# Kernel tuning notes

Hardware: AMD Instinct MI355X
Metric: run time of the kernel (lower is better)

The kernel has to match this reference:

```python
import jax, jax.numpy as jnp
import numpy as np

B, NQ, NP, C, H = 8, 1024, 2048, 1024, 16
D = C // H  # head_dim = 64


def setup_inputs() -> dict:
    key = jax.random.key(0)
    ks = jax.random.split(key, 12)
    s = 1.0 / np.sqrt(C)
    inp = {
        "x": jax.random.normal(ks[0], (B, NQ, C), dtype=jnp.float32),
        "ctx": jax.random.normal(ks[1], (B, NP, C), dtype=jnp.float32),
        "freqs_cis": jax.random.normal(ks[2], (NP, D // 2, 2), dtype=jnp.float32),
        "wq": jax.random.normal(ks[3], (C, C), dtype=jnp.float32) * s,
        "bq": jnp.zeros((C,), dtype=jnp.float32),
        "wk": jax.random.normal(ks[4], (C, C), dtype=jnp.float32) * s,
        "bk": jnp.zeros((C,), dtype=jnp.float32),
        "wv": jax.random.normal(ks[5], (C, C), dtype=jnp.float32) * s,
        "bv": jnp.zeros((C,), dtype=jnp.float32),
        "wo": jax.random.normal(ks[6], (C, C), dtype=jnp.float32) * s,
        "bo": jnp.zeros((C,), dtype=jnp.float32),
    }
    return inp


def _apply_rope(k, freqs_cis):
    # k: [B, Np, H, D]; freqs_cis: [Np, D//2, 2] (cos, sin)
    b, n, h, d = k.shape
    kp = k.reshape(b, n, h, d // 2, 2)  # adjacent-pair complex convention
    kr, ki = kp[..., 0], kp[..., 1]
    cos = freqs_cis[None, :, None, :, 0]
    sin = freqs_cis[None, :, None, :, 1]
    out_r = kr * cos - ki * sin
    out_i = kr * sin + ki * cos
    return jnp.stack([out_r, out_i], axis=-1).reshape(b, n, h, d)


def reference(x, ctx, freqs_cis, wq, bq, wk, bk, wv, bv, wo, bo):
    b, nq, c = x.shape
    npx = ctx.shape[1]
    q = (jnp.einsum('bsc,oc->bso', x, wq) + bq).reshape(b, nq, H, D)
    k = (jnp.einsum('bsc,oc->bso', ctx, wk) + bk).reshape(b, npx, H, D)
    v = (jnp.einsum('bsc,oc->bso', ctx, wv) + bv).reshape(b, npx, H, D)
    k = _apply_rope(k, freqs_cis)
    scale = 1.0 / jnp.sqrt(jnp.asarray(D, dtype=q.dtype))
    scores = jnp.einsum('bqhd,bkhd->bhqk', q, k) * scale
    attn = jax.nn.softmax(scores, axis=-1)
    out = jnp.einsum('bhqk,bkhd->bqhd', attn, v).reshape(b, nq, c)
    return jnp.einsum('bsc,oc->bso', out, wo) + bo
```

## Files before the change

### kernel.cpp

```cpp
#include <hip/hip_runtime.h>
#include <stdint.h>

typedef __bf16 bf16;
typedef bf16 bf16x8 __attribute__((ext_vector_type(8)));
typedef float f32x4 __attribute__((ext_vector_type(4)));
typedef float f32x16 __attribute__((ext_vector_type(16)));
typedef uint32_t u32x4 __attribute__((ext_vector_type(4)));

static __device__ __forceinline__ void async_cp16(const bf16* gsrc, bf16* ldst) {
  __builtin_amdgcn_global_load_lds(
      (const __attribute__((address_space(1))) uint32_t*)gsrc,
      (__attribute__((address_space(3))) uint32_t*)ldst, 16, 0, 0);
}

static __device__ __forceinline__ f32x16 mfma32(bf16x8 a, bf16x8 b, f32x16 c) {
  return __builtin_amdgcn_mfma_f32_32x32x16_bf16(a, b, c, 0, 0, 0);
}

static __device__ __forceinline__ uint32_t cvtpk(float lo, float hi) {
  uint32_t r;
  asm("v_cvt_pk_bf16_f32 %0, %1, %2" : "=v"(r) : "v"(lo), "v"(hi));
  return r;
}
static __device__ __forceinline__ void plswap(uint32_t& a, uint32_t& b) {
  asm("v_permlane32_swap_b32 %0, %1" : "+v"(a), "+v"(b));
}

__global__ __launch_bounds__(256) void convert_all(
    const float* __restrict__ x, const float* __restrict__ ctx,
    const float* __restrict__ wq, const float* __restrict__ wk,
    const float* __restrict__ wv, const float* __restrict__ wo,
    bf16* __restrict__ xb, bf16* __restrict__ cb,
    bf16* __restrict__ wqb, bf16* __restrict__ wkb,
    bf16* __restrict__ wvb, bf16* __restrict__ wob) {
  int id = blockIdx.x;
  const float* s; bf16* d; int base;
  if (id < 8192)        { s = x;   d = xb;  base = id; }
  else if (id < 24576)  { s = ctx; d = cb;  base = id - 8192; }
  else if (id < 25600)  { s = wq;  d = wqb; base = id - 24576; }
  else if (id < 26624)  { s = wk;  d = wkb; base = id - 25600; }
  else if (id < 27648)  { s = wv;  d = wvb; base = id - 26624; }
  else                  { s = wo;  d = wob; base = id - 27648; }
  int i = base * 256 + threadIdx.x;
  float4 v = ((const float4*)s)[i];
  ushort4 o;
  o.x = __builtin_bit_cast(unsigned short, (bf16)v.x);
  o.y = __builtin_bit_cast(unsigned short, (bf16)v.y);
  o.z = __builtin_bit_cast(unsigned short, (bf16)v.z);
  o.w = __builtin_bit_cast(unsigned short, (bf16)v.w);
  ((ushort4*)d)[i] = o;
}

template <int OUT_F32>
__global__ __launch_bounds__(256) void gemm_bt(
    const bf16* __restrict__ A, const bf16* __restrict__ Bw,
    const float* __restrict__ bias, void* __restrict__ Cout,
    int M, int N, int K) {
  __shared__ __align__(16) bf16 sA[128 * 32];
  __shared__ __align__(16) bf16 sB[128 * 32];

  int per = gridDim.x >> 3;
  int id = blockIdx.x;
  int swz = (id & 7) * per + (id >> 3);
  int NB = N >> 7;
  int mb = swz / NB, nb = swz % NB;

  int t = threadIdx.x;
  int l = t & 63, w = t >> 6;
  int wr = (w >> 1) * 64, wc = (w & 1) * 64;
  int lr = l & 15, lk = (l >> 4) * 8;

  const bf16* Abase = A + (size_t)(mb * 128 + (t >> 2)) * K + (t & 3) * 8;
  const bf16* Bbase = Bw + (size_t)(nb * 128 + (t >> 2)) * K + (t & 3) * 8;
  bf16* ldsA = sA + w * 512;
  bf16* ldsB = sB + w * 512;

  f32x4 acc[4][4];
  for (int i = 0; i < 4; i++)
    for (int j = 0; j < 4; j++) acc[i][j] = f32x4{0.f, 0.f, 0.f, 0.f};

  for (int k0 = 0; k0 < K; k0 += 32) {
    async_cp16(Abase + k0, ldsA);
    async_cp16(Abase + k0 + (size_t)64 * K, ldsA + 2048);
    async_cp16(Bbase + k0, ldsB);
    async_cp16(Bbase + k0 + (size_t)64 * K, ldsB + 2048);
    __syncthreads();
    bf16x8 af[4], bfr[4];
    for (int mf = 0; mf < 4; mf++)
      af[mf] = *(const bf16x8*)&sA[(wr + mf * 16 + lr) * 32 + lk];
    for (int nf = 0; nf < 4; nf++)
      bfr[nf] = *(const bf16x8*)&sB[(wc + nf * 16 + lr) * 32 + lk];
    for (int mf = 0; mf < 4; mf++)
      for (int nf = 0; nf < 4; nf++)
        acc[mf][nf] = __builtin_amdgcn_mfma_f32_16x16x32_bf16(
            af[mf], bfr[nf], acc[mf][nf], 0, 0, 0);
    __syncthreads();
  }

  int row0 = mb * 128 + wr + (l >> 4) * 4;
  int col0 = nb * 128 + wc + lr;
  for (int nf = 0; nf < 4; nf++) {
    float bi = bias[col0 + nf * 16];
    for (int mf = 0; mf < 4; mf++)
      for (int j = 0; j < 4; j++) {
        int r = row0 + mf * 16 + j;
        int c = col0 + nf * 16;
        float v = acc[mf][nf][j] + bi;
        if (OUT_F32)
          ((float*)Cout)[(size_t)r * N + c] = v;
        else
          ((bf16*)Cout)[(size_t)r * N + c] = (bf16)v;
      }
  }
}

__global__ __launch_bounds__(256) void rope_k(bf16* __restrict__ kb,
                                              const float* __restrict__ freqs) {
  int g = blockIdx.x * 256 + threadIdx.x;
  int c8 = g & 7;
  int n = (g >> 7) & 2047;
  uint4 kv = ((const uint4*)kb)[g];
  const float* f = freqs + n * 64 + c8 * 8;
  float4 f0 = *(const float4*)f;
  float4 f1 = *(const float4*)(f + 4);
  float cs[4] = {f0.x, f0.z, f1.x, f1.z};
  float sn[4] = {f0.y, f0.w, f1.y, f1.z};
  sn[3] = f1.w;
  unsigned short* ks = (unsigned short*)&kv;
  uint4 out;
  unsigned short* os = (unsigned short*)&out;
  for (int p = 0; p < 4; p++) {
    float kr = (float)__builtin_bit_cast(bf16, ks[2 * p]);
    float ki = (float)__builtin_bit_cast(bf16, ks[2 * p + 1]);
    float orr = kr * cs[p] - ki * sn[p];
    float oii = kr * sn[p] + ki * cs[p];
    os[2 * p] = __builtin_bit_cast(unsigned short, (bf16)orr);
    os[2 * p + 1] = __builtin_bit_cast(unsigned short, (bf16)oii);
  }
  ((uint4*)kb)[g] = out;
}

__global__ __launch_bounds__(256) void attn_fwd(
    const bf16* __restrict__ Q, const bf16* __restrict__ Kb,
    const bf16* __restrict__ Vb, bf16* __restrict__ O) {
  __shared__ __align__(16) bf16 sK[2][4096];
  __shared__ __align__(16) bf16 sV[2][4096];

  int nblk = blockIdx.x;
  int bh = (nblk & 7) * 16 + (nblk >> 6);
  int qt = (nblk >> 3) & 7;
  int b = bh >> 4, h = bh & 15;

  int t = threadIdx.x, l = t & 63, w = t >> 6;
  int ln = l & 31, hi = l >> 5;

  int qg = qt * 128 + w * 32 + ln;
  const bf16* qp = Q + ((size_t)(b * 1024 + qg) * 16 + h) * 64 + hi * 8;
  bf16x8 qf[4];
#pragma unroll
  for (int ds = 0; ds < 4; ds++) qf[ds] = *(const bf16x8*)(qp + ds * 16);

  const bf16* kbase = Kb + ((size_t)b * 2048 * 16 + h) * 64;
  const bf16* vbase = Vb + ((size_t)b * 2048 * 16 + h) * 64;

  int krow = w * 8 + (l >> 3);
  int vr2 = t >> 3;
  int vc = t & 7;

  auto stageK = [&](int kv0, int nb) {
    int cg1 = (((l & 7) ^ (krow & 7) ^ ((krow >> 3) & 7))) * 8;
    int r2 = krow + 32;
    int cg2 = (((l & 7) ^ (r2 & 7) ^ ((r2 >> 3) & 7))) * 8;
    async_cp16(kbase + (size_t)(kv0 + krow) * 1024 + cg1, &sK[nb][w * 512]);
    async_cp16(kbase + (size_t)(kv0 + r2) * 1024 + cg2, &sK[nb][2048 + w * 512]);
  };

  uint4 vA, vB;
  auto loadV = [&](int kv0) {
    const bf16* s = vbase + (size_t)(kv0 + 2 * vr2) * 1024 + vc * 8;
    vA = *(const uint4*)s;
    vB = *(const uint4*)(s + 1024);
  };
  auto writeV = [&](int nb) {
    const uint32_t* a0 = (const uint32_t*)&vA;
    const uint32_t* a1 = (const uint32_t*)&vB;
#pragma unroll
    for (int i = 0; i < 8; i++) {
      uint32_t lo = (a0[i >> 1] >> ((i & 1) * 16)) & 0xffffu;
      uint32_t hw = (a1[i >> 1] >> ((i & 1) * 16)) & 0xffffu;
      int d = vc * 8 + i;
      int off = d * 64 + ((2 * vr2) ^ ((i ^ vc) << 3));
      *(uint32_t*)&sV[nb][off] = lo | (hw << 16);
    }
  };

  f32x16 o0, o1, s0, s1;
#pragma unroll
  for (int i = 0; i < 16; i++) { o0[i] = 0.f; o1[i] = 0.f; }
  float m_r = -1e30f, l_r = 0.f;
  const float K2 = 0.18033688011112042f;

  stageK(0, 0);
  loadV(0);
  writeV(0);
  __syncthreads();
  int cur = 0;

  int x0 = ((ln & 7) ^ (ln >> 3)) << 3;
  int x1 = x0 ^ (4 << 3);

  for (int tt = 0; tt < 32; tt++) {
    if (tt < 31) { stageK(tt * 64 + 64, cur ^ 1); loadV(tt * 64 + 64); }

#pragma unroll
    for (int i = 0; i < 16; i++) { s0[i] = 0.f; s1[i] = 0.f; }
    __builtin_amdgcn_s_setprio(1);
#pragma unroll
    for (int ds = 0; ds < 4; ds++) {
      int boff = ds * 16 + hi * 8;
      bf16x8 kf0 = *(const bf16x8*)&sK[cur][ln * 64 + (boff ^ x0)];
      bf16x8 kf1 = *(const bf16x8*)&sK[cur][(ln + 32) * 64 + (boff ^ x1)];
      s0 = mfma32(kf0, qf[ds], s0);
      s1 = mfma32(kf1, qf[ds], s1);
    }
    __builtin_amdgcn_s_setprio(0);

    float mx[16];
#pragma unroll
    for (int i = 0; i < 16; i++) mx[i] = fmaxf(s0[i], s1[i]);
#pragma unroll
    for (int st = 8; st >= 1; st >>= 1)
#pragma unroll
      for (int i = 0; i < st; i++) mx[i] = fmaxf(mx[i], mx[i + st]);
    float pmax = fmaxf(mx[0], __shfl_xor(mx[0], 32, 64));

    if (__any(pmax > m_r + 40.f)) {
      float mnew = fmaxf(m_r, pmax);
      float corr = __builtin_amdgcn_exp2f((m_r - mnew) * K2);
      m_r = mnew;
      l_r *= corr;
#pragma unroll
      for (int i = 0; i < 16; i++) { o0[i] *= corr; o1[i] *= corr; }
    }
    float mk = m_r * K2;
    float sm[16];
#pragma unroll
    for (int i = 0; i < 16; i++) {
      s0[i] = __builtin_amdgcn_exp2f(__builtin_fmaf(s0[i], K2, -mk));
      s1[i] = __builtin_amdgcn_exp2f(__builtin_fmaf(s1[i], K2, -mk));
      sm[i] = s0[i] + s1[i];
    }
#pragma unroll
    for (int st = 8; st >= 1; st >>= 1)
#pragma unroll
      for (int i = 0; i < st; i++) sm[i] += sm[i + st];
    l_r += sm[0] + __shfl_xor(sm[0], 32, 64);

    bf16x8 pa[4];
    auto mkfrags = [&](const f32x16& sv, int base) {
#pragma unroll
      for (int u = 0; u < 2; u++) {
        uint32_t w0a = cvtpk(sv[8 * u + 0], sv[8 * u + 1]);
        uint32_t w0b = cvtpk(sv[8 * u + 4], sv[8 * u + 5]);
        plswap(w0a, w0b);
        uint32_t w1a = cvtpk(sv[8 * u + 2], sv[8 * u + 3]);
        uint32_t w1b = cvtpk(sv[8 * u + 6], sv[8 * u + 7]);
        plswap(w1a, w1b);
        u32x4 tmp;
        tmp[0] = w0a; tmp[1] = w1a; tmp[2] = w0b; tmp[3] = w1b;
        pa[base + u] = __builtin_bit_cast(bf16x8, tmp);
      }
    };
    mkfrags(s0, 0);
    mkfrags(s1, 2);

    __builtin_amdgcn_s_setprio(1);
#pragma unroll
    for (int ks = 0; ks < 4; ks++) {
      int koff = ks * 16 + hi * 8;
      bf16x8 vf0 = *(const bf16x8*)&sV[cur][ln * 64 + (koff ^ x0)];
      bf16x8 vf1 = *(const bf16x8*)&sV[cur][(ln + 32) * 64 + (koff ^ x1)];
      o0 = mfma32(vf0, pa[ks], o0);
      o1 = mfma32(vf1, pa[ks], o1);
    }
    __builtin_amdgcn_s_setprio(0);

    if (tt < 31) writeV(cur ^ 1);
    __syncthreads();
    cur ^= 1;
  }

  float inv = __builtin_amdgcn_rcpf(l_r);
  bf16* obase = O + ((size_t)(b * 1024 + qt * 128 + w * 32 + ln) * 16 + h) * 64;
#pragma unroll
  for (int g = 0; g < 4; g++) {
    ushort4 p0, p1;
    p0.x = __builtin_bit_cast(unsigned short, (bf16)(o0[4 * g + 0] * inv));
    p0.y = __builtin_bit_cast(unsigned short, (bf16)(o0[4 * g + 1] * inv));
    p0.z = __builtin_bit_cast(unsigned short, (bf16)(o0[4 * g + 2] * inv));
    p0.w = __builtin_bit_cast(unsigned short, (bf16)(o0[4 * g + 3] * inv));
    p1.x = __builtin_bit_cast(unsigned short, (bf16)(o1[4 * g + 0] * inv));
    p1.y = __builtin_bit_cast(unsigned short, (bf16)(o1[4 * g + 1] * inv));
    p1.z = __builtin_bit_cast(unsigned short, (bf16)(o1[4 * g + 2] * inv));
    p1.w = __builtin_bit_cast(unsigned short, (bf16)(o1[4 * g + 3] * inv));
    *(ushort4*)&obase[8 * g + 4 * hi] = p0;
    *(ushort4*)&obase[32 + 8 * g + 4 * hi] = p1;
  }
}

extern "C" void kernel_launch(void* const* d_in, const int* in_sizes, int n_in,
                              void* d_out, int out_size, void* d_ws, size_t ws_size,
                              hipStream_t stream) {
  const float* x     = (const float*)d_in[0];
  const float* ctx   = (const float*)d_in[1];
  const float* freqs = (const float*)d_in[2];
  const float* wq    = (const float*)d_in[3];
  const float* bq    = (const float*)d_in[4];
  const float* wk    = (const float*)d_in[5];
  const float* bk    = (const float*)d_in[6];
  const float* wv    = (const float*)d_in[7];
  const float* bv    = (const float*)d_in[8];
  const float* wo    = (const float*)d_in[9];
  const float* bo    = (const float*)d_in[10];

  char* p = (char*)d_ws;
  bf16* xb  = (bf16*)p; p += (size_t)8192 * 1024 * 2;
  bf16* cb  = (bf16*)p; p += (size_t)16384 * 1024 * 2;
  bf16* wqb = (bf16*)p; p += (size_t)1024 * 1024 * 2;
  bf16* wkb = (bf16*)p; p += (size_t)1024 * 1024 * 2;
  bf16* wvb = (bf16*)p; p += (size_t)1024 * 1024 * 2;
  bf16* wob = (bf16*)p; p += (size_t)1024 * 1024 * 2;
  bf16* qb  = (bf16*)p; p += (size_t)8192 * 1024 * 2;
  bf16* kb  = (bf16*)p; p += (size_t)16384 * 1024 * 2;
  bf16* vb  = (bf16*)p; p += (size_t)16384 * 1024 * 2;
  bf16* ob  = xb;

  convert_all<<<28672, 256, 0, stream>>>(x, ctx, wq, wk, wv, wo,
                                         xb, cb, wqb, wkb, wvb, wob);
  gemm_bt<0><<<512, 256, 0, stream>>>(xb, wqb, bq, qb, 8192, 1024, 1024);
  gemm_bt<0><<<1024, 256, 0, stream>>>(cb, wkb, bk, kb, 16384, 1024, 1024);
  gemm_bt<0><<<1024, 256, 0, stream>>>(cb, wvb, bv, vb, 16384, 1024, 1024);
  rope_k<<<8192, 256, 0, stream>>>(kb, freqs);
  attn_fwd<<<1024, 256, 0, stream>>>(qb, kb, vb, ob);
  gemm_bt<1><<<512, 256, 0, stream>>>(ob, wob, bo, d_out, 8192, 1024, 1024);
}
```

Baseline: 332.8 us.

## Produce V transposed from projection GEMM and stage it asynchronously in attention

The V projection GEMM now computes Wv·ctxᵀ, so V is written transposed ([C, B*NP]) with the bias added per row. The attention kernel then loads V tiles with the same async global-to-LDS swizzled copies used for K. This removes the register load, in-register transpose and scattered LDS writes of V from the inner loop. In exchange the V GEMM's output store is strided across 16384 columns, and the GEMM tile swizzle now runs over a grid with 8 row blocks and 128 column blocks.

```diff
diff --git a/kernel.cpp b/kernel.cpp
--- a/kernel.cpp
+++ b/kernel.cpp
@@ -51,7 +51,7 @@
   ((ushort4*)d)[i] = o;
 }
 
-template <int OUT_F32>
+template <int OUT_F32, int BIAS_ROW = 0>
 __global__ __launch_bounds__(256) void gemm_bt(
     const bf16* __restrict__ A, const bf16* __restrict__ Bw,
     const float* __restrict__ bias, void* __restrict__ Cout,
@@ -100,12 +100,12 @@
   int row0 = mb * 128 + wr + (l >> 4) * 4;
   int col0 = nb * 128 + wc + lr;
   for (int nf = 0; nf < 4; nf++) {
-    float bi = bias[col0 + nf * 16];
+    float bi = BIAS_ROW ? 0.f : bias[col0 + nf * 16];
     for (int mf = 0; mf < 4; mf++)
       for (int j = 0; j < 4; j++) {
         int r = row0 + mf * 16 + j;
         int c = col0 + nf * 16;
-        float v = acc[mf][nf][j] + bi;
+        float v = acc[mf][nf][j] + (BIAS_ROW ? bias[r] : bi);
         if (OUT_F32)
           ((float*)Cout)[(size_t)r * N + c] = v;
         else
@@ -142,7 +142,7 @@
 
 __global__ __launch_bounds__(256) void attn_fwd(
     const bf16* __restrict__ Q, const bf16* __restrict__ Kb,
-    const bf16* __restrict__ Vb, bf16* __restrict__ O) {
+    const bf16* __restrict__ VT, bf16* __restrict__ O) {
   __shared__ __align__(16) bf16 sK[2][4096];
   __shared__ __align__(16) bf16 sV[2][4096];
 
@@ -161,37 +161,20 @@
   for (int ds = 0; ds < 4; ds++) qf[ds] = *(const bf16x8*)(qp + ds * 16);
 
   const bf16* kbase = Kb + ((size_t)b * 2048 * 16 + h) * 64;
-  const bf16* vbase = Vb + ((size_t)b * 2048 * 16 + h) * 64;
+  const bf16* vtbase = VT + (size_t)(h * 64) * 16384 + b * 2048;
 
   int krow = w * 8 + (l >> 3);
-  int vr2 = t >> 3;
-  int vc = t & 7;
+  int cg1 = ((l & 7) ^ (krow & 7) ^ ((krow >> 3) & 7)) * 8;
+  int r2 = krow + 32;
+  int cg2 = ((l & 7) ^ (r2 & 7) ^ ((r2 >> 3) & 7)) * 8;
 
   auto stageK = [&](int kv0, int nb) {
-    int cg1 = (((l & 7) ^ (krow & 7) ^ ((krow >> 3) & 7))) * 8;
-    int r2 = krow + 32;
-    int cg2 = (((l & 7) ^ (r2 & 7) ^ ((r2 >> 3) & 7))) * 8;
     async_cp16(kbase + (size_t)(kv0 + krow) * 1024 + cg1, &sK[nb][w * 512]);
     async_cp16(kbase + (size_t)(kv0 + r2) * 1024 + cg2, &sK[nb][2048 + w * 512]);
   };
-
-  uint4 vA, vB;
-  auto loadV = [&](int kv0) {
-    const bf16* s = vbase + (size_t)(kv0 + 2 * vr2) * 1024 + vc * 8;
-    vA = *(const uint4*)s;
-    vB = *(const uint4*)(s + 1024);
-  };
-  auto writeV = [&](int nb) {
-    const uint32_t* a0 = (const uint32_t*)&vA;
-    const uint32_t* a1 = (const uint32_t*)&vB;
-#pragma unroll
-    for (int i = 0; i < 8; i++) {
-      uint32_t lo = (a0[i >> 1] >> ((i & 1) * 16)) & 0xffffu;
-      uint32_t hw = (a1[i >> 1] >> ((i & 1) * 16)) & 0xffffu;
-      int d = vc * 8 + i;
-      int off = d * 64 + ((2 * vr2) ^ ((i ^ vc) << 3));
-      *(uint32_t*)&sV[nb][off] = lo | (hw << 16);
-    }
+  auto stageV = [&](int kv0, int nb) {
+    async_cp16(vtbase + (size_t)krow * 16384 + kv0 + cg1, &sV[nb][w * 512]);
+    async_cp16(vtbase + (size_t)r2 * 16384 + kv0 + cg2, &sV[nb][2048 + w * 512]);
   };
 
   f32x16 o0, o1, s0, s1;
@@ -201,8 +184,7 @@
   const float K2 = 0.18033688011112042f;
 
   stageK(0, 0);
-  loadV(0);
-  writeV(0);
+  stageV(0, 0);
   __syncthreads();
   int cur = 0;
 
@@ -210,7 +192,7 @@
   int x1 = x0 ^ (4 << 3);
 
   for (int tt = 0; tt < 32; tt++) {
-    if (tt < 31) { stageK(tt * 64 + 64, cur ^ 1); loadV(tt * 64 + 64); }
+    if (tt < 31) { stageK(tt * 64 + 64, cur ^ 1); stageV(tt * 64 + 64, cur ^ 1); }
 
 #pragma unroll
     for (int i = 0; i < 16; i++) { s0[i] = 0.f; s1[i] = 0.f; }
@@ -285,7 +267,6 @@
     }
     __builtin_amdgcn_s_setprio(0);
 
-    if (tt < 31) writeV(cur ^ 1);
     __syncthreads();
     cur ^= 1;
   }
@@ -332,15 +313,15 @@
   bf16* wob = (bf16*)p; p += (size_t)1024 * 1024 * 2;
   bf16* qb  = (bf16*)p; p += (size_t)8192 * 1024 * 2;
   bf16* kb  = (bf16*)p; p += (size_t)16384 * 1024 * 2;
-  bf16* vb  = (bf16*)p; p += (size_t)16384 * 1024 * 2;
+  bf16* vt  = (bf16*)p; p += (size_t)16384 * 1024 * 2;
   bf16* ob  = xb;
 
   convert_all<<<28672, 256, 0, stream>>>(x, ctx, wq, wk, wv, wo,
                                          xb, cb, wqb, wkb, wvb, wob);
   gemm_bt<0><<<512, 256, 0, stream>>>(xb, wqb, bq, qb, 8192, 1024, 1024);
   gemm_bt<0><<<1024, 256, 0, stream>>>(cb, wkb, bk, kb, 16384, 1024, 1024);
-  gemm_bt<0><<<1024, 256, 0, stream>>>(cb, wvb, bv, vb, 16384, 1024, 1024);
+  gemm_bt<0, 1><<<1024, 256, 0, stream>>>(wvb, cb, bv, vt, 1024, 16384, 1024);
   rope_k<<<8192, 256, 0, stream>>>(kb, freqs);
-  attn_fwd<<<1024, 256, 0, stream>>>(qb, kb, vb, ob);
+  attn_fwd<<<1024, 256, 0, stream>>>(qb, kb, vt, ob);
   gemm_bt<1><<<512, 256, 0, stream>>>(ob, wob, bo, d_out, 8192, 1024, 1024);
 }
```

Result: faster. 322.3 us (-3.2%).
